# Kernel optimization log

Hardware: AMD Instinct MI355X
Metric: run time of the kernel (lower is better)

The kernel has to match this reference:

```python
import jax, jax.numpy as jnp
import numpy as np

N_NODES = 100000
N_EDGES = 1600000
STATE_DIM = 5
EDGE_FEAT = 8
MAX_ITER = 50
THRESH = 0.01


def setup_inputs() -> dict:
    key = jax.random.key(0)
    ks = jax.random.split(key, 12)
    s = 0.2  # small init scale to keep tanh unsaturated
    return {
        "edge_feat": jax.random.normal(ks[0], (N_EDGES, EDGE_FEAT), jnp.float32),
        "edge_src": jax.random.randint(ks[1], (N_EDGES,), 0, N_NODES, jnp.int32),
        "arc_rows": jax.random.randint(ks[2], (N_EDGES,), 0, N_NODES, jnp.int32),
        "arc_vals": jax.random.uniform(ks[3], (N_EDGES,), jnp.float32),
        "state_init": jnp.zeros((N_NODES, STATE_DIM), jnp.float32),
        "old_state_init": jnp.ones((N_NODES, STATE_DIM), jnp.float32),
        "W1": jax.random.normal(ks[4], (EDGE_FEAT + STATE_DIM, 15), jnp.float32) * s,
        "b1": jnp.zeros((15,), jnp.float32),
        "W2": jax.random.normal(ks[5], (15, STATE_DIM), jnp.float32) * s,
        "b2": jnp.zeros((STATE_DIM,), jnp.float32),
        "W3": jax.random.normal(ks[6], (STATE_DIM, 10), jnp.float32) * s,
        "b3": jnp.zeros((10,), jnp.float32),
        "W4": jax.random.normal(ks[7], (10, 7), jnp.float32) * s,
        "b4": jnp.zeros((7,), jnp.float32),
    }


def reference(edge_feat, edge_src, arc_rows, arc_vals,
              state_init, old_state_init,
              W1, b1, W2, b2, W3, b3, W4, b4):
    def step(carry, _):
        state, old, k = carry
        # while_loop condition evaluated on current carry
        dist = jnp.sqrt(jnp.sum(jnp.square(state - old), axis=1) + 1e-11)
        cond = jnp.logical_and(jnp.any(dist > THRESH), k < MAX_ITER)
        # body: gather node states by edge index, concat edge features, tiny MLP
        gat = state[edge_src]                              # [E, 5]
        inp = jnp.concatenate([edge_feat, gat], axis=1)    # [E, 13]
        h1 = jnp.tanh(inp @ W1 + b1)                       # [E, 15]
        h2 = jnp.tanh(h1 @ W2 + b2)                        # [E, 5]
        # ArcNode sparse-dense matmul == weighted scatter-add of edges into nodes
        new_state = jax.ops.segment_sum(h2 * arc_vals[:, None], arc_rows,
                                        num_segments=N_NODES)  # [N, 5]
        state_n = jnp.where(cond, new_state, state)
        old_n = jnp.where(cond, state, old)
        k_n = k + cond.astype(jnp.int32)
        return (state_n, old_n, k_n), None

    k0 = jnp.asarray(0, jnp.int32)
    (st, _, num), _ = jax.lax.scan(step, (state_init, old_state_init, k0),
                                   None, length=MAX_ITER)
    out1 = jnp.tanh(st @ W3 + b3)                          # [N, 10]
    out = jax.nn.softmax(out1 @ W4 + b4, axis=-1)          # [N, 7]
    return out, num
```

## Files before the change

kernel.cpp:

```cpp
#include <hip/hip_runtime.h>
#include <hip/hip_fp16.h>
#include <math.h>

#define N_NODES 100000
#define N_EDGES 1600000
#define MAX_ITER 50
#define THRESH 0.01f
#define SCAN_CHUNK 1024
#define NBLK_SCAN 98
#define NB_EDGE ((N_EDGES + 255) / 256)
#define WAVES_TOTAL 3125
#define BLK_PIPE 782


__device__ __forceinline__ float fast_tanh(float x) {
    float ax = fabsf(x);
    float e = __expf(2.0f * ax);
    float r = 1.0f - 2.0f * __builtin_amdgcn_rcpf(e + 1.0f);
    return copysignf(r, x);
}

__global__ void zero_ints(int* p, int n) {
    int i = blockIdx.x * blockDim.x + threadIdx.x;
    if (i < n) p[i] = 0;
}

__global__ void zero_floats(float* p, int n) {
    int i = blockIdx.x * blockDim.x + threadIdx.x;
    if (i < n) p[i] = 0.f;
}

__global__ void hist_kernel(const int* __restrict__ rows, int* __restrict__ cnt) {
    int e = blockIdx.x * blockDim.x + threadIdx.x;
    if (e < N_EDGES) atomicAdd(&cnt[rows[e]], 1);
}

__global__ __launch_bounds__(256) void scan1_kernel(const int* __restrict__ cnt,
                                                    int* __restrict__ off,
                                                    int* __restrict__ bsum) {
    __shared__ int sm[256];
    int b = blockIdx.x, t = threadIdx.x;
    int base = b * SCAN_CHUNK + t * 4;
    int v[4];
    int tsum = 0;
#pragma unroll
    for (int j = 0; j < 4; ++j) {
        v[j] = (base + j < N_NODES) ? cnt[base + j] : 0;
        tsum += v[j];
    }
    int val = tsum;
    sm[t] = val;
    __syncthreads();
    for (int d = 1; d < 256; d <<= 1) {
        int x = (t >= d) ? sm[t - d] : 0;
        __syncthreads();
        val += x;
        sm[t] = val;
        __syncthreads();
    }
    int run = val - tsum;
#pragma unroll
    for (int j = 0; j < 4; ++j) {
        if (base + j < N_NODES) off[base + j] = run;
        run += v[j];
    }
    if (t == 255) bsum[b] = val;
}

__global__ __launch_bounds__(128) void scan2_kernel(int* __restrict__ bsum) {
    __shared__ int sm[128];
    int t = threadIdx.x;
    int v = (t < NBLK_SCAN) ? bsum[t] : 0;
    int val = v;
    sm[t] = val;
    __syncthreads();
    for (int d = 1; d < 128; d <<= 1) {
        int x = (t >= d) ? sm[t - d] : 0;
        __syncthreads();
        val += x;
        sm[t] = val;
        __syncthreads();
    }
    if (t < NBLK_SCAN) bsum[t] = val - v;
}

__global__ __launch_bounds__(256) void scan3_kernel(int* __restrict__ off,
                                                    const int* __restrict__ bsum) {
    int b = blockIdx.x, t = threadIdx.x;
    int add = bsum[b];
    int base = b * SCAN_CHUNK + t * 4;
#pragma unroll
    for (int j = 0; j < 4; ++j)
        if (base + j < N_NODES) off[base + j] += add;
    if (b == 0 && t == 0) off[N_NODES] = N_EDGES;
}

__global__ void scatter_perm(const int* __restrict__ rows,
                             const int* __restrict__ off,
                             int* __restrict__ cur,
                             int* __restrict__ perm) {
    int e = blockIdx.x * blockDim.x + threadIdx.x;
    if (e >= N_EDGES) return;
    int r = rows[e];
    int p = off[r] + atomicAdd(&cur[r], 1);
    perm[p] = e;
}

__global__ void wprep_kernel(const float* __restrict__ W1, const float* __restrict__ b1,
                             const float* __restrict__ W2, const float* __restrict__ b2,
                             float* __restrict__ wc) {
    int t = threadIdx.x;
    for (int idx = t; idx < 75; idx += 256) { int j = idx / 5, i = idx % 5; wc[idx] = W1[(8 + i) * 15 + j]; }
    for (int idx = t; idx < 75; idx += 256) { int j = idx / 15, i = idx % 15; wc[75 + idx] = W2[i * 5 + j]; }
    for (int idx = t; idx < 5; idx += 256) wc[150 + idx] = b2[idx];
    for (int idx = t; idx < 120; idx += 256) { int j = idx / 8, i = idx % 8; wc[160 + idx] = W1[i * 15 + j]; }
    for (int idx = t; idx < 15; idx += 256) wc[280 + idx] = b1[idx];
}

union RecPack { __half2 h2[8]; uint4 u4[2]; };
union U4H { uint4 u; __half2 h[4]; };

__global__ __launch_bounds__(256) void build_rec(
    const int* __restrict__ perm, const int* __restrict__ rows,
    const int* __restrict__ esrc, const float* __restrict__ avals,
    const float* __restrict__ efeat, const float* __restrict__ wc,
    uint4* __restrict__ c1h, int2* __restrict__ sv, int* __restrict__ rowsg) {
    int p = blockIdx.x * blockDim.x + threadIdx.x;
    if (p >= N_EDGES) return;
    int e = perm[p];
    const float4* fp = (const float4*)(efeat + (size_t)e * 8);
    float4 f0 = fp[0], f1 = fp[1];
    const float* W1F = wc + 160;
    const float* B1 = wc + 280;
    float c[15];
#pragma unroll
    for (int j = 0; j < 15; ++j) {
        float a = B1[j];
        a += f0.x * W1F[j * 8 + 0] + f0.y * W1F[j * 8 + 1] + f0.z * W1F[j * 8 + 2] + f0.w * W1F[j * 8 + 3];
        a += f1.x * W1F[j * 8 + 4] + f1.y * W1F[j * 8 + 5] + f1.z * W1F[j * 8 + 6] + f1.w * W1F[j * 8 + 7];
        c[j] = a;
    }
    RecPack rp;
#pragma unroll
    for (int j = 0; j < 7; ++j) rp.h2[j] = __floats2half2_rn(c[2 * j], c[2 * j + 1]);
    rp.h2[7] = __floats2half2_rn(c[14], 0.f);
    c1h[2 * p] = rp.u4[0];
    c1h[2 * p + 1] = rp.u4[1];
    sv[p] = make_int2(esrc[e], __float_as_int(avals[e]));
    rowsg[p] = rows[e];
}

__global__ void init_state8_kernel(const float* __restrict__ state_init,
                                   const float* __restrict__ old_init,
                                   float* __restrict__ buf0,
                                   int* __restrict__ flags) {
    int n = blockIdx.x * blockDim.x + threadIdx.x;
    if (n >= N_NODES) return;
    float ss = 0.f;
    float s[5];
#pragma unroll
    for (int j = 0; j < 5; ++j) {
        s[j] = state_init[n * 5 + j];
        float d = s[j] - old_init[n * 5 + j];
        ss += d * d;
    }
    ((float4*)(buf0 + (size_t)n * 8))[0] = make_float4(s[0], s[1], s[2], s[3]);
    ((float4*)(buf0 + (size_t)n * 8))[1] = make_float4(s[4], 0.f, 0.f, 0.f);
    int pred = sqrtf(ss + 1e-11f) > THRESH;
    unsigned long long m = __ballot(pred);
    if ((threadIdx.x & 63) == 0 && m) atomicOr(&flags[0], 1);
}

__global__ __launch_bounds__(256) void edge_pipe_kernel(
    const int* __restrict__ rowsg, const uint4* __restrict__ c1h,
    const int2* __restrict__ sv,
    const float* __restrict__ sprev, float* __restrict__ snext,
    const float* __restrict__ wc, const int* __restrict__ flag_cur) {
    if (*flag_cur == 0) return;
    int gtid = blockIdx.x * 256 + threadIdx.x;
    int wid = gtid >> 6;
    int lane = threadIdx.x & 63;
    if (wid >= WAVES_TOTAL) return;
    int base = wid * 512;

    int head_prev = (wid > 0) ? rowsg[base - 1] : -2;
    int tail_next = (wid < WAVES_TOTAL - 1) ? rowsg[base + 512] : -2;

    const float* W1S = wc;
    const float* W2T = wc + 75;
    const float* B2  = wc + 150;

    int carry_row = -1;
    bool carry_head = false;
    float cv0 = 0, cv1 = 0, cv2 = 0, cv3 = 0, cv4 = 0;

    int p0 = base + lane;
    uint4 a0 = c1h[2 * p0];
    uint4 a1 = c1h[2 * p0 + 1];
    int2 svv = sv[p0];
    int rr = rowsg[p0];

    for (int k = 0; k < 8; ++k) {
        uint4 b0 = a0, b1 = a1;
        int2 s = svv;
        int r = rr;
        if (k < 7) {
            int np = base + (k + 1) * 64 + lane;
            a0 = c1h[2 * np];
            a1 = c1h[2 * np + 1];
            svv = sv[np];
            rr = rowsg[np];
        }
        float4 st0 = ((const float4*)(sprev + (size_t)s.x * 8))[0];
        float st4 = sprev[(size_t)s.x * 8 + 4];
        float av = __int_as_float(s.y);
        U4H ua, ub;
        ua.u = b0; ub.u = b1;
        float c1[15];
#pragma unroll
        for (int j = 0; j < 4; ++j) {
            float2 f = __half22float2(ua.h[j]);
            c1[2 * j] = f.x; c1[2 * j + 1] = f.y;
        }
#pragma unroll
        for (int j = 0; j < 3; ++j) {
            float2 f = __half22float2(ub.h[j]);
            c1[8 + 2 * j] = f.x; c1[9 + 2 * j] = f.y;
        }
        c1[14] = __half22float2(ub.h[3]).x;
        float h1[15];
#pragma unroll
        for (int j = 0; j < 15; ++j) {
            float a = c1[j];
            a += st0.x * W1S[j * 5 + 0];
            a += st0.y * W1S[j * 5 + 1];
            a += st0.z * W1S[j * 5 + 2];
            a += st0.w * W1S[j * 5 + 3];
            a += st4  * W1S[j * 5 + 4];
            h1[j] = fast_tanh(a);
        }
        float v0, v1, v2, v3, v4;
        {
            float o[5];
#pragma unroll
            for (int j = 0; j < 5; ++j) {
                float a = B2[j];
#pragma unroll
                for (int i = 0; i < 15; ++i) a += h1[i] * W2T[j * 15 + i];
                o[j] = fast_tanh(a) * av;
            }
            v0 = o[0]; v1 = o[1]; v2 = o[2]; v3 = o[3]; v4 = o[4];
        }
#pragma unroll
        for (int d = 1; d < 64; d <<= 1) {
            int pr = __shfl_up(r, d, 64);
            float t0 = __shfl_up(v0, d, 64);
            float t1 = __shfl_up(v1, d, 64);
            float t2 = __shfl_up(v2, d, 64);
            float t3 = __shfl_up(v3, d, 64);
            float t4 = __shfl_up(v4, d, 64);
            if (lane >= d && pr == r) { v0 += t0; v1 += t1; v2 += t2; v3 += t3; v4 += t4; }
        }
        int rn = __shfl_down(r, 1, 64);
        int r_next_first = (k < 7) ? __shfl(rr, 0, 64) : -3;

        bool is_tail = (lane == 63) || (rn != r);
        float w0 = v0, w1 = v1, w2 = v2, w3 = v3, w4 = v4;
        if (is_tail && r == carry_row) { w0 += cv0; w1 += cv1; w2 += cv2; w3 += cv3; w4 += cv4; }
        bool rh = (r == carry_row && carry_head) || (k == 0 && head_prev == r);
        bool cont = is_tail && (lane == 63) && (k < 7) && (r == r_next_first);
        if (is_tail && !cont) {
            bool wec = (lane == 63) && (k == 7) && (r == tail_next);
            float* dst = snext + (size_t)r * 8;
            if (rh || wec) {
                atomicAdd(dst + 0, w0);
                atomicAdd(dst + 1, w1);
                atomicAdd(dst + 2, w2);
                atomicAdd(dst + 3, w3);
                atomicAdd(dst + 4, w4);
            } else {
                ((float4*)dst)[0] = make_float4(w0, w1, w2, w3);
                dst[4] = w4;
            }
        }
        int cont63 = __shfl((int)cont, 63, 64);
        int cr63 = __shfl(r, 63, 64);
        int ch63 = __shfl((int)rh, 63, 64);
        float nc0 = __shfl(w0, 63, 64);
        float nc1 = __shfl(w1, 63, 64);
        float nc2 = __shfl(w2, 63, 64);
        float nc3 = __shfl(w3, 63, 64);
        float nc4 = __shfl(w4, 63, 64);
        carry_row = cont63 ? cr63 : -1;
        carry_head = cont63 && ch63;
        cv0 = nc0; cv1 = nc1; cv2 = nc2; cv3 = nc3; cv4 = nc4;
    }
}

__global__ void node_pass_kernel(float* __restrict__ sp, float* __restrict__ sn,
                                 const int* __restrict__ flag_cur,
                                 int* __restrict__ flag_next,
                                 int* __restrict__ kcnt) {
    int n = blockIdx.x * blockDim.x + threadIdx.x;
    if (n >= N_NODES) return;
    bool active = (*flag_cur != 0);
    float4 o0 = ((const float4*)(sp + (size_t)n * 8))[0];
    float o4 = sp[(size_t)n * 8 + 4];
    int pred = 0;
    if (active) {
        if (n == 0) *kcnt += 1;
        float4 s0 = ((const float4*)(sn + (size_t)n * 8))[0];
        float s4 = sn[(size_t)n * 8 + 4];
        float d0 = s0.x - o0.x, d1 = s0.y - o0.y, d2 = s0.z - o0.z;
        float d3 = s0.w - o0.w, d4 = s4 - o4;
        float ss = d0 * d0 + d1 * d1 + d2 * d2 + d3 * d3 + d4 * d4;
        pred = sqrtf(ss + 1e-11f) > THRESH;
    } else {
        ((float4*)(sn + (size_t)n * 8))[0] = o0;
        sn[(size_t)n * 8 + 4] = o4;
    }
    ((float4*)(sp + (size_t)n * 8))[0] = make_float4(0.f, 0.f, 0.f, 0.f);
    sp[(size_t)n * 8 + 4] = 0.f;
    unsigned long long m = __ballot(pred);
    if ((threadIdx.x & 63) == 0 && m) atomicOr(flag_next, 1);
}

__global__ void final8_kernel(const float* __restrict__ state,
                              const float* __restrict__ W3, const float* __restrict__ b3,
                              const float* __restrict__ W4, const float* __restrict__ b4,
                              const int* __restrict__ kcnt,
                              float* __restrict__ out) {
    int n = blockIdx.x * blockDim.x + threadIdx.x;
    if (n == 0) out[(size_t)N_NODES * 7] = (float)(*kcnt);
    if (n >= N_NODES) return;
    float st[5];
    float4 s0 = ((const float4*)(state + (size_t)n * 8))[0];
    st[0] = s0.x; st[1] = s0.y; st[2] = s0.z; st[3] = s0.w;
    st[4] = state[(size_t)n * 8 + 4];
    float o1[10];
#pragma unroll
    for (int j = 0; j < 10; ++j) {
        float a = b3[j];
#pragma unroll
        for (int i = 0; i < 5; ++i) a += st[i] * W3[i * 10 + j];
        o1[j] = tanhf(a);
    }
    float z[7];
    float m = -1e30f;
#pragma unroll
    for (int j = 0; j < 7; ++j) {
        float a = b4[j];
#pragma unroll
        for (int i = 0; i < 10; ++i) a += o1[i] * W4[i * 7 + j];
        z[j] = a;
        m = fmaxf(m, a);
    }
    float s = 0.f;
#pragma unroll
    for (int j = 0; j < 7; ++j) { z[j] = expf(z[j] - m); s += z[j]; }
    float inv = 1.f / s;
#pragma unroll
    for (int j = 0; j < 7; ++j) out[(size_t)n * 7 + j] = z[j] * inv;
}

extern "C" void kernel_launch(void* const* d_in, const int* in_sizes, int n_in,
                              void* d_out, int out_size, void* d_ws, size_t ws_size,
                              hipStream_t stream) {
    const float* edge_feat  = (const float*)d_in[0];
    const int*   edge_src   = (const int*)d_in[1];
    const int*   arc_rows   = (const int*)d_in[2];
    const float* arc_vals   = (const float*)d_in[3];
    const float* state_init = (const float*)d_in[4];
    const float* old_init   = (const float*)d_in[5];
    const float* W1 = (const float*)d_in[6];
    const float* b1 = (const float*)d_in[7];
    const float* W2 = (const float*)d_in[8];
    const float* b2 = (const float*)d_in[9];
    const float* W3 = (const float*)d_in[10];
    const float* b3 = (const float*)d_in[11];
    const float* W4 = (const float*)d_in[12];
    const float* b4 = (const float*)d_in[13];

    char* ws = (char*)d_ws;
    int*   off   = (int*)(ws + 0);
    int*   cnt   = (int*)(ws + 400128);
    int*   flags = (int*)(ws + 800128);
    int*   kcnt  = flags + 51;
    float* wc    = (float*)(ws + 800384);
    float* buf0  = (float*)(ws + 801664);
    float* buf1  = (float*)(ws + 4001664);
    int*   perm  = (int*)(ws + 7201664);
    int*   rowsg = (int*)(ws + 13601664);
    uint4* c1h   = (uint4*)(ws + 20001664);
    int2*  sv    = (int2*)(ws + 71201664);
    int*   bsum  = (int*)(ws + 20001664);

    int nb = (N_NODES + 255) / 256;
    int eb = NB_EDGE;

    hipLaunchKernelGGL(zero_ints, dim3(nb), dim3(256), 0, stream, cnt, N_NODES);
    hipLaunchKernelGGL(zero_ints, dim3(1), dim3(64), 0, stream, flags, 52);
    hipLaunchKernelGGL(hist_kernel, dim3(eb), dim3(256), 0, stream, arc_rows, cnt);
    hipLaunchKernelGGL(scan1_kernel, dim3(NBLK_SCAN), dim3(256), 0, stream, cnt, off, bsum);
    hipLaunchKernelGGL(scan2_kernel, dim3(1), dim3(128), 0, stream, bsum);
    hipLaunchKernelGGL(scan3_kernel, dim3(NBLK_SCAN), dim3(256), 0, stream, off, bsum);
    hipLaunchKernelGGL(zero_ints, dim3(nb), dim3(256), 0, stream, cnt, N_NODES);
    hipLaunchKernelGGL(scatter_perm, dim3(eb), dim3(256), 0, stream, arc_rows, off, cnt, perm);
    hipLaunchKernelGGL(wprep_kernel, dim3(1), dim3(256), 0, stream, W1, b1, W2, b2, wc);
    hipLaunchKernelGGL(build_rec, dim3(eb), dim3(256), 0, stream,
                       perm, arc_rows, edge_src, arc_vals, edge_feat, wc, c1h, sv, rowsg);
    hipLaunchKernelGGL(init_state8_kernel, dim3(nb), dim3(256), 0, stream,
                       state_init, old_init, buf0, flags);
    hipLaunchKernelGGL(zero_floats, dim3((N_NODES * 8 + 255) / 256), dim3(256), 0, stream,
                       buf1, N_NODES * 8);

    for (int it = 0; it < MAX_ITER; ++it) {
        float* sp = (it & 1) ? buf1 : buf0;
        float* sn = (it & 1) ? buf0 : buf1;
        hipLaunchKernelGGL(edge_pipe_kernel, dim3(BLK_PIPE), dim3(256), 0, stream,
                           rowsg, c1h, sv, sp, sn, wc, flags + it);
        hipLaunchKernelGGL(node_pass_kernel, dim3(nb), dim3(256), 0, stream,
                           sp, sn, flags + it, flags + it + 1, kcnt);
    }

    hipLaunchKernelGGL(final8_kernel, dim3(nb), dim3(256), 0, stream,
                       buf0, W3, b3, W4, b4, kcnt, (float*)d_out);
}
```

Baseline: 3.430 ms.

## Fuse edge scatter into record build, deepen gather prefetch, ballot-based segmented scan

```diff
diff --git a/kernel.cpp b/kernel.cpp
--- a/kernel.cpp
+++ b/kernel.cpp
@@ -9,8 +9,10 @@
 #define SCAN_CHUNK 1024
 #define NBLK_SCAN 98
 #define NB_EDGE ((N_EDGES + 255) / 256)
-#define WAVES_TOTAL 3125
-#define BLK_PIPE 782
+#define SLOTS_W 320
+#define GROUPS 5
+#define WAVES_TOTAL 5000
+#define BLK_PIPE 1250
 
 
 __device__ __forceinline__ float fast_tanh(float x) {
@@ -95,17 +97,6 @@
     if (b == 0 && t == 0) off[N_NODES] = N_EDGES;
 }
 
-__global__ void scatter_perm(const int* __restrict__ rows,
-                             const int* __restrict__ off,
-                             int* __restrict__ cur,
-                             int* __restrict__ perm) {
-    int e = blockIdx.x * blockDim.x + threadIdx.x;
-    if (e >= N_EDGES) return;
-    int r = rows[e];
-    int p = off[r] + atomicAdd(&cur[r], 1);
-    perm[p] = e;
-}
-
 __global__ void wprep_kernel(const float* __restrict__ W1, const float* __restrict__ b1,
                              const float* __restrict__ W2, const float* __restrict__ b2,
                              float* __restrict__ wc) {
@@ -120,14 +111,16 @@
 union RecPack { __half2 h2[8]; uint4 u4[2]; };
 union U4H { uint4 u; __half2 h[4]; };
 
-__global__ __launch_bounds__(256) void build_rec(
-    const int* __restrict__ perm, const int* __restrict__ rows,
-    const int* __restrict__ esrc, const float* __restrict__ avals,
-    const float* __restrict__ efeat, const float* __restrict__ wc,
+__global__ __launch_bounds__(256) void scatter_build2(
+    const int* __restrict__ rows, const int* __restrict__ esrc,
+    const float* __restrict__ avals, const float* __restrict__ efeat,
+    const int* __restrict__ off, int* __restrict__ cur,
+    const float* __restrict__ wc,
     uint4* __restrict__ c1h, int2* __restrict__ sv, int* __restrict__ rowsg) {
-    int p = blockIdx.x * blockDim.x + threadIdx.x;
-    if (p >= N_EDGES) return;
-    int e = perm[p];
+    int e = blockIdx.x * blockDim.x + threadIdx.x;
+    if (e >= N_EDGES) return;
+    int r = rows[e];
+    int p = off[r] + atomicAdd(&cur[r], 1);
     const float4* fp = (const float4*)(efeat + (size_t)e * 8);
     float4 f0 = fp[0], f1 = fp[1];
     const float* W1F = wc + 160;
@@ -147,7 +140,7 @@
     c1h[2 * p] = rp.u4[0];
     c1h[2 * p + 1] = rp.u4[1];
     sv[p] = make_int2(esrc[e], __float_as_int(avals[e]));
-    rowsg[p] = rows[e];
+    rowsg[p] = r;
 }
 
 __global__ void init_state8_kernel(const float* __restrict__ state_init,
@@ -181,10 +174,10 @@
     int wid = gtid >> 6;
     int lane = threadIdx.x & 63;
     if (wid >= WAVES_TOTAL) return;
-    int base = wid * 512;
+    int base = wid * SLOTS_W;
 
     int head_prev = (wid > 0) ? rowsg[base - 1] : -2;
-    int tail_next = (wid < WAVES_TOTAL - 1) ? rowsg[base + 512] : -2;
+    int tail_next = (wid < WAVES_TOTAL - 1) ? rowsg[base + SLOTS_W] : -2;
 
     const float* W1S = wc;
     const float* W2T = wc + 75;
@@ -195,27 +188,29 @@
     float cv0 = 0, cv1 = 0, cv2 = 0, cv3 = 0, cv4 = 0;
 
     int p0 = base + lane;
-    uint4 a0 = c1h[2 * p0];
-    uint4 a1 = c1h[2 * p0 + 1];
-    int2 svv = sv[p0];
-    int rr = rowsg[p0];
-
-    for (int k = 0; k < 8; ++k) {
-        uint4 b0 = a0, b1 = a1;
-        int2 s = svv;
-        int r = rr;
-        if (k < 7) {
-            int np = base + (k + 1) * 64 + lane;
-            a0 = c1h[2 * np];
-            a1 = c1h[2 * np + 1];
-            svv = sv[np];
-            rr = rowsg[np];
-        }
-        float4 st0 = ((const float4*)(sprev + (size_t)s.x * 8))[0];
-        float st4 = sprev[(size_t)s.x * 8 + 4];
-        float av = __int_as_float(s.y);
+    int2 s0m = sv[p0];            int r0v = rowsg[p0];
+    int2 s1m = sv[p0 + 64];       int r1v = rowsg[p0 + 64];
+    float4 g0a = ((const float4*)(sprev + (size_t)s0m.x * 8))[0];
+    float  g0b = sprev[(size_t)s0m.x * 8 + 4];
+    uint4 c0a = c1h[2 * p0], c0b = c1h[2 * p0 + 1];
+
+    for (int k = 0; k < GROUPS; ++k) {
+        int2 s2m; int r2v;
+        if (k + 2 < GROUPS) {
+            int p2 = base + (k + 2) * 64 + lane;
+            s2m = sv[p2]; r2v = rowsg[p2];
+        }
+        float4 g1a; float g1b; uint4 c1a, c1b;
+        if (k + 1 < GROUPS) {
+            int p1 = base + (k + 1) * 64 + lane;
+            g1a = ((const float4*)(sprev + (size_t)s1m.x * 8))[0];
+            g1b = sprev[(size_t)s1m.x * 8 + 4];
+            c1a = c1h[2 * p1]; c1b = c1h[2 * p1 + 1];
+        }
+        int r = r0v;
+        float av = __int_as_float(s0m.y);
         U4H ua, ub;
-        ua.u = b0; ub.u = b1;
+        ua.u = c0a; ub.u = c0b;
         float c1[15];
 #pragma unroll
         for (int j = 0; j < 4; ++j) {
@@ -232,11 +227,11 @@
 #pragma unroll
         for (int j = 0; j < 15; ++j) {
             float a = c1[j];
-            a += st0.x * W1S[j * 5 + 0];
-            a += st0.y * W1S[j * 5 + 1];
-            a += st0.z * W1S[j * 5 + 2];
-            a += st0.w * W1S[j * 5 + 3];
-            a += st4  * W1S[j * 5 + 4];
+            a += g0a.x * W1S[j * 5 + 0];
+            a += g0a.y * W1S[j * 5 + 1];
+            a += g0a.z * W1S[j * 5 + 2];
+            a += g0a.w * W1S[j * 5 + 3];
+            a += g0b  * W1S[j * 5 + 4];
             h1[j] = fast_tanh(a);
         }
         float v0, v1, v2, v3, v4;
@@ -251,26 +246,30 @@
             }
             v0 = o[0]; v1 = o[1]; v2 = o[2]; v3 = o[3]; v4 = o[4];
         }
+        int rprev = __shfl_up(r, 1, 64);
+        bool head = (lane == 0) || (rprev != r);
+        unsigned long long hm = __ballot(head);
+        unsigned long long below = hm & (0xFFFFFFFFFFFFFFFFULL >> (63 - lane));
+        int segstart = 63 - __clzll(below);
 #pragma unroll
         for (int d = 1; d < 64; d <<= 1) {
-            int pr = __shfl_up(r, d, 64);
             float t0 = __shfl_up(v0, d, 64);
             float t1 = __shfl_up(v1, d, 64);
             float t2 = __shfl_up(v2, d, 64);
             float t3 = __shfl_up(v3, d, 64);
             float t4 = __shfl_up(v4, d, 64);
-            if (lane >= d && pr == r) { v0 += t0; v1 += t1; v2 += t2; v3 += t3; v4 += t4; }
-        }
-        int rn = __shfl_down(r, 1, 64);
-        int r_next_first = (k < 7) ? __shfl(rr, 0, 64) : -3;
-
-        bool is_tail = (lane == 63) || (rn != r);
+            if (lane - d >= segstart) { v0 += t0; v1 += t1; v2 += t2; v3 += t3; v4 += t4; }
+        }
+        bool next_head = (lane < 63) && ((hm >> (lane + 1)) & 1ULL);
+        bool is_tail = (lane == 63) || next_head;
+        int r_next_first = (k + 1 < GROUPS) ? __shfl(r1v, 0, 64) : -3;
+
         float w0 = v0, w1 = v1, w2 = v2, w3 = v3, w4 = v4;
         if (is_tail && r == carry_row) { w0 += cv0; w1 += cv1; w2 += cv2; w3 += cv3; w4 += cv4; }
         bool rh = (r == carry_row && carry_head) || (k == 0 && head_prev == r);
-        bool cont = is_tail && (lane == 63) && (k < 7) && (r == r_next_first);
+        bool cont = is_tail && (lane == 63) && (k + 1 < GROUPS) && (r == r_next_first);
         if (is_tail && !cont) {
-            bool wec = (lane == 63) && (k == 7) && (r == tail_next);
+            bool wec = (lane == 63) && (k == GROUPS - 1) && (r == tail_next);
             float* dst = snext + (size_t)r * 8;
             if (rh || wec) {
                 atomicAdd(dst + 0, w0);
@@ -294,6 +293,8 @@
         carry_row = cont63 ? cr63 : -1;
         carry_head = cont63 && ch63;
         cv0 = nc0; cv1 = nc1; cv2 = nc2; cv3 = nc3; cv4 = nc4;
+        s0m = s1m; r0v = r1v; g0a = g1a; g0b = g1b; c0a = c1a; c0b = c1b;
+        s1m = s2m; r1v = r2v;
     }
 }
 
@@ -389,11 +390,10 @@
     float* wc    = (float*)(ws + 800384);
     float* buf0  = (float*)(ws + 801664);
     float* buf1  = (float*)(ws + 4001664);
-    int*   perm  = (int*)(ws + 7201664);
-    int*   rowsg = (int*)(ws + 13601664);
-    uint4* c1h   = (uint4*)(ws + 20001664);
-    int2*  sv    = (int2*)(ws + 71201664);
-    int*   bsum  = (int*)(ws + 20001664);
+    int*   rowsg = (int*)(ws + 7201664);
+    int2*  sv    = (int2*)(ws + 13601664);
+    uint4* c1h   = (uint4*)(ws + 26401664);
+    int*   bsum  = (int*)(ws + 26401664);
 
     int nb = (N_NODES + 255) / 256;
     int eb = NB_EDGE;
@@ -405,10 +405,9 @@
     hipLaunchKernelGGL(scan2_kernel, dim3(1), dim3(128), 0, stream, bsum);
     hipLaunchKernelGGL(scan3_kernel, dim3(NBLK_SCAN), dim3(256), 0, stream, off, bsum);
     hipLaunchKernelGGL(zero_ints, dim3(nb), dim3(256), 0, stream, cnt, N_NODES);
-    hipLaunchKernelGGL(scatter_perm, dim3(eb), dim3(256), 0, stream, arc_rows, off, cnt, perm);
     hipLaunchKernelGGL(wprep_kernel, dim3(1), dim3(256), 0, stream, W1, b1, W2, b2, wc);
-    hipLaunchKernelGGL(build_rec, dim3(eb), dim3(256), 0, stream,
-                       perm, arc_rows, edge_src, arc_vals, edge_feat, wc, c1h, sv, rowsg);
+    hipLaunchKernelGGL(scatter_build2, dim3(eb), dim3(256), 0, stream,
+                       arc_rows, edge_src, arc_vals, edge_feat, off, cnt, wc, c1h, sv, rowsg);
     hipLaunchKernelGGL(init_state8_kernel, dim3(nb), dim3(256), 0, stream,
                        state_init, old_init, buf0, flags);
     hipLaunchKernelGGL(zero_floats, dim3((N_NODES * 8 + 255) / 256), dim3(256), 0, stream,
```

Result: faster. 3.161 ms (-7.8%).
